# Optimization experiments

Hardware: AMD Instinct MI355X
Metric: run time of the kernel (lower is better)

The kernel has to match this reference:

```python
import jax, jax.numpy as jnp
import numpy as np

N, H, LAT, V = 256, 450, 56, 780  # nodes, hidden_size, latent_size, vocab_size


def _build_tree(seed=0):
    """Random tree on N nodes + DFS path matching the torch dfs() (children in ascending id order)."""
    rng = np.random.default_rng(seed)
    children = [[] for _ in range(N)]
    for i in range(1, N):
        children[int(rng.integers(0, i))].append(i)
    path = []
    stack = [(0, 0)]
    while stack:
        u, ci = stack.pop()
        ch = children[u]
        if ci < len(ch):
            stack.append((u, ci + 1))
            path.append((u, 1))   # descend to child -> stop flag 1
            stack.append((ch[ci], 0))
        else:
            path.append((u, 0))   # backtrack -> stop flag 0
    return path


def setup_inputs() -> dict:
    key = jax.random.key(0)
    ks = jax.random.split(key, 18)
    path = _build_tree()
    L = len(path)  # 2N-1 = 511
    node_ids = np.array([p[0] for p in path], dtype=np.int32)
    stops = np.array([p[1] for p in path], dtype=np.int32)
    next_ids = np.concatenate([node_ids[1:], np.zeros(1, np.int32)])
    label_steps = np.where(stops == 1)[0].astype(np.int32)  # N-1 steps that emit a label
    rng = np.random.default_rng(1)
    vids = rng.integers(0, V, size=N).astype(np.int32)
    node_feature = np.zeros((N, V), np.float32)
    node_feature[np.arange(N), vids] = 1.0  # one-hot vocab features, as in JT-VAE
    real_labels = np.concatenate([vids[:1], vids[next_ids[label_steps]]]).astype(np.int32)  # [N]
    w = lambda k, shape: (jax.random.normal(k, shape, jnp.float32) * 0.05)
    return {
        "latent_code": jax.random.normal(ks[0], (LAT,), jnp.float32),
        "node_feature": jnp.asarray(node_feature),
        "node_ids": jnp.asarray(node_ids),
        "next_ids": jnp.asarray(next_ids),
        "stops": jnp.asarray(stops),
        "label_steps": jnp.asarray(label_steps),
        "real_labels": jnp.asarray(real_labels),
        "Wz_w": w(ks[1], (H, V + H)), "Wz_b": w(ks[2], (H,)),
        "Ur_w": w(ks[3], (H, H)),
        "Wr_w": w(ks[4], (H, V)), "Wr_b": w(ks[5], (H,)),
        "Wh_w": w(ks[6], (H, V + H)), "Wh_b": w(ks[7], (H,)),
        "Wd12_w": w(ks[8], (H, V + LAT)), "Wd12_b": w(ks[9], (H,)),
        "Wd3_w": w(ks[10], (H, H)), "Wd3_b": w(ks[11], (H,)),
        "Ud_w": w(ks[12], (1, 2 * H)), "Ud_b": w(ks[13], (1,)),
        "Wl_w": w(ks[14], (H, H + LAT)), "Wl_b": w(ks[15], (H,)),
        "Ul_w": w(ks[16], (V, H)), "Ul_b": w(ks[17], (V,)),
    }


def reference(latent_code, node_feature, node_ids, next_ids, stops, label_steps, real_labels,
              Wz_w, Wz_b, Ur_w, Wr_w, Wr_b, Wh_w, Wh_b, Wd12_w, Wd12_b, Wd3_w, Wd3_b,
              Ud_w, Ud_b, Wl_w, Wl_b, Ul_w, Ul_b):
    n = node_feature.shape[0]
    h = Wz_w.shape[0]
    L = node_ids.shape[0]

    # Root label: F.relu(U_l(W_l(cat(latent, zeros(h)))))  -- relu OUTSIDE U_l, no softmax.
    root_in = jnp.concatenate([latent_code, jnp.zeros((h,), latent_code.dtype)])
    root_label = jax.nn.relu((root_in @ Wl_w.T + Wl_b) @ Ul_w.T + Ul_b)

    def step(carry, xs):
        hidden, enc = carry            # hidden: [n,n,h], enc: [n,n]
        a, b, is_last = xs
        x = node_feature[a]            # [V] one-hot row
        hs = hidden[:, a]              # [n,h] incoming messages into node a
        # Stop prediction (uses pre-update hidden)
        d12 = jnp.concatenate([x, latent_code]) @ Wd12_w.T + Wd12_b
        d3 = hs.sum(0) @ Wd3_w.T + Wd3_b
        pred_stop = (jax.nn.relu(jnp.concatenate([d12, d3])) @ Ud_w.T + Ud_b)[0]
        # GRU message a -> b, excluding the edge (a,b) from the neighbor mask
        enc0 = enc.at[a, b].set(0.0).at[b, a].set(0.0)
        mask = enc0[:, a]              # [n]
        Hm = hs * mask[:, None]        # masked gathered hidden
        s = Hm.sum(0)                  # [h]
        z = jax.nn.sigmoid(jnp.concatenate([x, s]) @ Wz_w.T + Wz_b)
        r1 = x @ Wr_w.T + Wr_b         # [h]
        r = jax.nn.sigmoid(r1 + Hm @ Ur_w.T)  # [n,h]; torch sums sigmoid over ALL n rows
        gated = jnp.tanh(jnp.concatenate([x, r.sum(0)]) @ Wh_w.T + Wh_b)
        new_h = (1.0 - z) * s + z * gated
        hidden_new = hidden.at[a, b].set(new_h)
        enc_new = enc0.at[a, b].set(1.0).at[b, a].set(1.0)
        hidden = jnp.where(is_last, hidden, hidden_new)  # last path entry: break before update
        enc = jnp.where(is_last, enc, enc_new)
        # Child label: softmax(U_l(relu(W_l(cat(latent, new_h)))))  -- relu INSIDE, then softmax
        lab_in = jnp.concatenate([latent_code, new_h])
        label = jax.nn.softmax(jax.nn.relu(lab_in @ Wl_w.T + Wl_b) @ Ul_w.T + Ul_b)
        return (hidden, enc), (pred_stop, label)

    hidden0 = jnp.zeros((n, n, h), jnp.float32)
    enc0 = jnp.zeros((n, n), jnp.float32)
    is_last = jnp.arange(L) == (L - 1)
    (_, _), (pred_stops, labels) = jax.lax.scan(step, (hidden0, enc0), (node_ids, next_ids, is_last))
    pred_labels = jnp.concatenate([root_label[None], labels[label_steps]], axis=0)  # [N, V]
    return stops.astype(jnp.float32), pred_stops, real_labels, pred_labels
```

## Files before the change

### kernel.cpp

```cpp
#include <hip/hip_runtime.h>
#include <math.h>

#define NN   256
#define HH   450
#define LATD 56
#define VV   780
#define LL   511
#define GSEQ 32
#define TSEQ 512
#define KMAX 15
#define AST  16

typedef float f8 __attribute__((ext_vector_type(8)));

__device__ __forceinline__ float wred_sum(float v) {
    for (int off = 32; off; off >>= 1) v += __shfl_down(v, off, 64);
    return v;
}

__device__ __forceinline__ void aadd(float* p, float v) {
    (void)__hip_atomic_fetch_add(p, v, __ATOMIC_RELAXED, __HIP_MEMORY_SCOPE_AGENT);
}
__device__ __forceinline__ void ast64(unsigned long long* p, unsigned long long v) {
    __hip_atomic_store(p, v, __ATOMIC_RELAXED, __HIP_MEMORY_SCOPE_AGENT);
}
__device__ __forceinline__ unsigned long long ald64(const unsigned long long* p) {
    return __hip_atomic_load(p, __ATOMIC_RELAXED, __HIP_MEMORY_SCOPE_AGENT);
}
__device__ __forceinline__ unsigned long long pk64(float v, unsigned tag) {
    return ((unsigned long long)tag << 32) | (unsigned long long)__float_as_uint(v);
}
__device__ __forceinline__ float lo32f(unsigned long long x) { return __uint_as_float((unsigned)x); }
__device__ __forceinline__ unsigned hi32(unsigned long long x) { return (unsigned)(x >> 32); }

__global__ void k_vid(const float* __restrict__ nf, int* __restrict__ vid) {
    const int u = blockIdx.x;
    for (int v = threadIdx.x; v < VV; v += blockDim.x)
        if (nf[(size_t)u * VV + v] > 0.5f) vid[u] = v;
}

__global__ __launch_bounds__(512) void k_consts(
    const int* __restrict__ vid, const float* __restrict__ latent,
    const float* __restrict__ Wz, const float* __restrict__ Wzb,
    const float* __restrict__ Wr, const float* __restrict__ Wrb,
    const float* __restrict__ Wh, const float* __restrict__ Whb,
    const float* __restrict__ Wd12, const float* __restrict__ Wd12b,
    const float* __restrict__ Ud,
    float* __restrict__ cz, float* __restrict__ r1s, float* __restrict__ sig0,
    float* __restrict__ ch, float* __restrict__ dotd12)
{
    const int u = blockIdx.x, tid = threadIdx.x;
    const int v = vid[u];
    __shared__ float red[8];
    float p = 0.f;
    if (tid < HH) {
        const int i = tid, o = u * HH + i;
        cz[o] = Wz[(size_t)i * (VV + HH) + v] + Wzb[i];
        const float r1 = Wr[(size_t)i * VV + v] + Wrb[i];
        r1s[o] = r1;
        sig0[o] = 1.f / (1.f + expf(-r1));
        ch[o] = Wh[(size_t)i * (VV + HH) + v] + Whb[i];
        float d = Wd12[(size_t)i * (VV + LATD) + v] + Wd12b[i];
        for (int k = 0; k < LATD; ++k)
            d += Wd12[(size_t)i * (VV + LATD) + VV + k] * latent[k];
        p = Ud[i] * fmaxf(d, 0.f);
    }
    p = wred_sum(p);
    if ((tid & 63) == 0) red[tid >> 6] = p;
    __syncthreads();
    if (tid == 0) {
        float s = 0.f;
        for (int w = 0; w < 8; ++w) s += red[w];
        dotd12[u] = s;
    }
}

__global__ __launch_bounds__(512) void k_whsig0(
    const float* __restrict__ Wh, const float* __restrict__ sig0, float* __restrict__ out)
{
    const int u = blockIdx.x, tid = threadIdx.x, wave = tid >> 6, lane = tid & 63;
    __shared__ float sg[HH];
    if (tid < HH) sg[tid] = sig0[u * HH + tid];
    __syncthreads();
    for (int r = wave; r < HH; r += 8) {
        float acc = 0.f;
        for (int k = lane; k < HH; k += 64)
            acc += Wh[(size_t)r * (VV + HH) + VV + k] * sg[k];
        acc = wred_sum(acc);
        if (lane == 0) out[u * HH + r] = acc;
    }
}

__global__ void k_excl(const int* __restrict__ node_ids, const int* __restrict__ next_ids,
                       int* __restrict__ excl, float* __restrict__ ccpre)
{
    const int t = blockIdx.x;
    __shared__ int ex, cnt;
    if (threadIdx.x == 0) { ex = -1; cnt = 0; }
    __syncthreads();
    const int a = node_ids[t], b = next_ids[t];
    for (int tp = threadIdx.x; tp <= t; tp += blockDim.x) {
        if (tp < t && node_ids[tp] == b && next_ids[tp] == a) ex = tp;
        if (tp >= 1 && node_ids[tp] == a) atomicAdd(&cnt, 1);
    }
    __syncthreads();
    if (threadIdx.x == 0) {
        excl[t] = ex;
        ccpre[t] = 256.f - (float)cnt + (ex >= 0 ? 1.f : 0.f);
    }
}

__global__ void k_copy(const int* __restrict__ stops, const int* __restrict__ reall,
                       float* __restrict__ out)
{
    const int i = blockIdx.x * blockDim.x + threadIdx.x;
    if (i < LL) { out[i] = (float)stops[i]; out[LL + i] = 0.f; }
    if (i < NN) out[2 * LL + i] = (float)reall[i];
}

__global__ __launch_bounds__(TSEQ) void k_seq(
    const int* __restrict__ node_ids, const int* __restrict__ excl,
    const float* __restrict__ ccpre,
    const float* __restrict__ Ur, const float* __restrict__ Wz,
    const float* __restrict__ Wh, const float* __restrict__ Wd3,
    const float* __restrict__ Wd3b, const float* __restrict__ Ud,
    const float* __restrict__ Udb,
    const float* __restrict__ cz, const float* __restrict__ r1s,
    const float* __restrict__ ch, const float* __restrict__ WhSig0,
    const float* __restrict__ dotd12,
    float* __restrict__ Wd3SmL,
    float* __restrict__ NewHL, float* __restrict__ WzML, float* __restrict__ WhSvL,
    unsigned long long* __restrict__ bcNh, unsigned long long* __restrict__ bcSig,
    float* __restrict__ pred_out)
{
    const int tid = threadIdx.x, bid = blockIdx.x;
    const int wave = tid >> 6, lane = tid & 63;
    const int kcnt = 14 + (bid < 2 ? 1 : 0);
    const int kbeg = 14 * bid + (bid < 2 ? bid : 2);

    float* myWd3S = Wd3SmL + (size_t)bid * NN * AST;
    float* myNewH = NewHL  + (size_t)bid * LL * AST;
    float* myWzM  = WzML   + (size_t)bid * LL * AST;
    float* myWhSv = WhSvL  + (size_t)bid * LL * AST;

    __shared__ float sSm[NN * AST];
    __shared__ float sWzSm[NN * AST];
    __shared__ float sWhRs[NN * AST];
    __shared__ float nh_full[512];
    __shared__ float sig_full[512];
    __shared__ float sNhR[4][AST];
    __shared__ float sWzR[4][AST];
    __shared__ float sWhR[4][AST];

    f8 urw[2], wzw[2], wd3w[2], whw[2];
    #pragma unroll
    for (int it = 0; it < 2; ++it) {
        const int j = wave + 8 * it;
        const bool vj = j < kcnt;
        const int r = vj ? (kbeg + j) : 0;
        #pragma unroll
        for (int e = 0; e < 8; ++e) {
            const int c = lane + 64 * e;
            const bool vc = vj && (c < HH);
            urw[it][e]  = vc ? Ur[(size_t)r * HH + c] : 0.f;
            wzw[it][e]  = vc ? Wz[(size_t)r * (VV + HH) + VV + c] : 0.f;
            wd3w[it][e] = vc ? Wd3[(size_t)r * HH + c] : 0.f;
            whw[it][e]  = vc ? Wh[(size_t)r * (VV + HH) + VV + c] : 0.f;
        }
    }
    float ud_r = 0.f, w3b_r = 0.f;
    if (tid < kcnt) { ud_r = Ud[HH + kbeg + tid]; w3b_r = Wd3b[kbeg + tid]; }
    const float udb0 = Udb[0];

    for (int i = tid; i < NN * AST; i += TSEQ) { sSm[i] = 0.f; sWzSm[i] = 0.f; sWhRs[i] = 0.f; }
    nh_full[tid] = 0.f; sig_full[tid] = 0.f;

    int ap = node_ids[0];
    float pcz = 0.f, pch = 0.f, pws = 0.f;
    if (tid < kcnt) {
        const int o = ap * HH + kbeg + tid;
        pcz = cz[o]; pch = ch[o]; pws = WhSig0[o];
    }
    float pcc = ccpre[0];
    int  pidx = excl[0];
    __syncthreads();

    for (int t = 1; t <= LL; ++t) {
        const int idx = pidx;
        float nh = 0.f;
        if (tid < kcnt) {
            const int oa = ap * AST + tid;
            float zarg = sWzSm[oa] + pcz;
            float whv  = sWhRs[oa] + pch;
            float sv   = sSm[oa];
            if (idx >= 0) {
                float enh, ewz, ewh;
                if (idx >= t - 4) {
                    const int sl = idx & 3;
                    enh = sNhR[sl][tid]; ewz = sWzR[sl][tid]; ewh = sWhR[sl][tid];
                } else {
                    const int oe = idx * AST + tid;
                    enh = myNewH[oe]; ewz = myWzM[oe]; ewh = myWhSv[oe];
                }
                zarg -= ewz; whv -= ewh; sv -= enh;
            }
            whv += pcc * pws;
            const float z = 1.f / (1.f + expf(-zarg));
            nh = (1.f - z) * sv + z * tanhf(whv);
            if (t < LL)
                ast64(&bcNh[(size_t)((t & 1) * 512 + kbeg + tid)], pk64(nh, (unsigned)t));
            myNewH[(t - 1) * AST + tid] = nh;
            sNhR[(t - 1) & 3][tid] = nh;
        }
        if (wave == 0) {
            float ps = 0.f;
            if (tid < kcnt)
                ps = ud_r * fmaxf(myWd3S[ap * AST + tid] + w3b_r, 0.f);
            ps = wred_sum(ps);
            if (lane == 0) {
                if (bid == 0) ps += dotd12[ap] + udb0;
                aadd(&pred_out[t - 1], ps);
            }
        }
        if (t == LL) break;
        const int a = node_ids[t];
        const unsigned tag = (unsigned)t;
        const int p = t & 1;

        float r1v[2];
        #pragma unroll
        for (int it = 0; it < 2; ++it) {
            const int j = wave + 8 * it;
            r1v[it] = r1s[(size_t)a * HH + ((j < kcnt) ? (kbeg + j) : 0)];
        }
        if (tid < kcnt) sSm[a * AST + tid] += nh;

        if (tid < HH) {
            const unsigned long long* pp = &bcNh[(size_t)(p * 512 + tid)];
            unsigned long long e = ald64(pp);
            while (hi32(e) != tag) { __builtin_amdgcn_s_sleep(1); e = ald64(pp); }
            nh_full[tid] = lo32f(e);
        }
        __syncthreads();

        #pragma unroll
        for (int it = 0; it < 2; ++it) {
            const int j = wave + 8 * it;
            float acc = 0.f;
            #pragma unroll
            for (int e = 0; e < 8; ++e) acc += urw[it][e] * nh_full[lane + 64 * e];
            acc = wred_sum(acc);
            if (lane == 0 && j < kcnt) {
                const float sg = 1.f / (1.f + expf(-(acc + r1v[it])));
                ast64(&bcSig[(size_t)(p * 512 + kbeg + j)], pk64(sg, tag));
            }
        }

        #pragma unroll
        for (int it = 0; it < 2; ++it) {
            const int j = wave + 8 * it;
            float az = 0.f, ad = 0.f;
            #pragma unroll
            for (int e = 0; e < 8; ++e) {
                const float x = nh_full[lane + 64 * e];
                az += wzw[it][e] * x;
                ad += wd3w[it][e] * x;
            }
            az = wred_sum(az); ad = wred_sum(ad);
            if (lane == 0 && j < kcnt) {
                myWzM[(t - 1) * AST + j] = az;
                sWzR[(t - 1) & 3][j] = az;
                sWzSm[a * AST + j] += az;
                myWd3S[a * AST + j] += ad;
            }
        }
        if (tid < kcnt) {
            const int o = a * HH + kbeg + tid;
            pcz = cz[o]; pch = ch[o]; pws = WhSig0[o];
        }
        pcc = ccpre[t]; pidx = excl[t];

        if (tid < HH) {
            const unsigned long long* pp = &bcSig[(size_t)(p * 512 + tid)];
            unsigned long long e = ald64(pp);
            while (hi32(e) != tag) { __builtin_amdgcn_s_sleep(1); e = ald64(pp); }
            sig_full[tid] = lo32f(e);
        }
        __syncthreads();

        #pragma unroll
        for (int it = 0; it < 2; ++it) {
            const int j = wave + 8 * it;
            float aw = 0.f;
            #pragma unroll
            for (int e = 0; e < 8; ++e) aw += whw[it][e] * sig_full[lane + 64 * e];
            aw = wred_sum(aw);
            if (lane == 0 && j < kcnt) {
                myWhSv[(t - 1) * AST + j] = aw;
                sWhR[(t - 1) & 3][j] = aw;
                sWhRs[a * AST + j] += aw;
            }
        }
        ap = a;
        __syncthreads();
    }
}

__global__ __launch_bounds__(512) void k_label(
    const float* __restrict__ latent, const int* __restrict__ lsteps,
    const float* __restrict__ NewHL,
    const float* __restrict__ Wl, const float* __restrict__ Wlb,
    const float* __restrict__ Ul, const float* __restrict__ Ulb,
    float* __restrict__ out)
{
    const int q = blockIdx.x, tid = threadIdx.x, wave = tid >> 6, lane = tid & 63;
    __shared__ float inp[LATD + HH];
    __shared__ float t2[HH];
    __shared__ float lg[VV];
    __shared__ float red[8];
    if (tid < LATD) inp[tid] = latent[tid];
    if (q == 0) {
        if (tid < HH) inp[LATD + tid] = 0.f;
    } else {
        const int t = lsteps[q - 1];
        if (tid < HH) {
            const int b = (tid < 30) ? (tid / 15) : (2 + (tid - 30) / 14);
            const int j = (tid < 30) ? (tid % 15) : ((tid - 30) % 14);
            inp[LATD + tid] = NewHL[((size_t)b * LL + t) * AST + j];
        }
    }
    __syncthreads();
    for (int r = wave; r < HH; r += 8) {
        float acc = 0.f;
        for (int k = lane; k < LATD + HH; k += 64)
            acc += Wl[(size_t)r * (LATD + HH) + k] * inp[k];
        acc = wred_sum(acc);
        if (lane == 0) {
            const float v = acc + Wlb[r];
            t2[r] = (q == 0) ? v : fmaxf(v, 0.f);
        }
    }
    __syncthreads();
    for (int r = wave; r < VV; r += 8) {
        float acc = 0.f;
        for (int k = lane; k < HH; k += 64) acc += Ul[(size_t)r * HH + k] * t2[k];
        acc = wred_sum(acc);
        if (lane == 0) lg[r] = acc + Ulb[r];
    }
    __syncthreads();
    float* outrow = out + 2 * LL + NN + (size_t)q * VV;
    if (q == 0) {
        for (int i = tid; i < VV; i += 512) outrow[i] = fmaxf(lg[i], 0.f);
        return;
    }
    float mx = -1e30f;
    for (int i = tid; i < VV; i += 512) mx = fmaxf(mx, lg[i]);
    for (int off = 32; off; off >>= 1) mx = fmaxf(mx, __shfl_down(mx, off, 64));
    if (lane == 0) red[wave] = mx;
    __syncthreads();
    if (tid == 0) {
        float m = red[0];
        for (int w = 1; w < 8; ++w) m = fmaxf(m, red[w]);
        red[0] = m;
    }
    __syncthreads();
    const float M = red[0];
    float sum = 0.f;
    for (int i = tid; i < VV; i += 512) { const float e = expf(lg[i] - M); lg[i] = e; sum += e; }
    __syncthreads();
    sum = wred_sum(sum);
    if (lane == 0) red[wave] = sum;
    __syncthreads();
    if (tid == 0) {
        float s = 0.f;
        for (int w = 0; w < 8; ++w) s += red[w];
        red[0] = s;
    }
    __syncthreads();
    const float S = red[0];
    for (int i = tid; i < VV; i += 512) outrow[i] = lg[i] / S;
}

extern "C" void kernel_launch(void* const* d_in, const int* in_sizes, int n_in,
                              void* d_out, int out_size, void* d_ws, size_t ws_size,
                              hipStream_t stream)
{
    const float* latent = (const float*)d_in[0];
    const float* nodef  = (const float*)d_in[1];
    const int* node_ids = (const int*)d_in[2];
    const int* next_ids = (const int*)d_in[3];
    const int* stops    = (const int*)d_in[4];
    const int* lsteps   = (const int*)d_in[5];
    const int* reall    = (const int*)d_in[6];
    const float* Wz   = (const float*)d_in[7];
    const float* Wzb  = (const float*)d_in[8];
    const float* Urw  = (const float*)d_in[9];
    const float* Wr   = (const float*)d_in[10];
    const float* Wrb  = (const float*)d_in[11];
    const float* Wh   = (const float*)d_in[12];
    const float* Whb  = (const float*)d_in[13];
    const float* Wd12 = (const float*)d_in[14];
    const float* Wd12b= (const float*)d_in[15];
    const float* Wd3  = (const float*)d_in[16];
    const float* Wd3b = (const float*)d_in[17];
    const float* Ud   = (const float*)d_in[18];
    const float* Udb  = (const float*)d_in[19];
    const float* Wl   = (const float*)d_in[20];
    const float* Wlb  = (const float*)d_in[21];
    const float* Ul   = (const float*)d_in[22];
    const float* Ulb  = (const float*)d_in[23];
    (void)in_sizes; (void)n_in; (void)out_size; (void)ws_size;
    float* out = (float*)d_out;
    float* W = (float*)d_ws;

    size_t o = 0;
    float* Wd3SmL = W + o; o += (size_t)GSEQ * NN * AST;
    unsigned long long* bcNh  = (unsigned long long*)(W + o); o += 2 * 512 * 2;
    unsigned long long* bcSig = (unsigned long long*)(W + o); o += 2 * 512 * 2;
    const size_t zero_floats = o;
    int*   vid    = (int*)(W + o); o += NN;
    int*   excl   = (int*)(W + o); o += LL + 1;
    float* ccpre  = W + o; o += LL + 1;
    float* cz     = W + o; o += NN * HH;
    float* r1s    = W + o; o += NN * HH;
    float* sig0   = W + o; o += NN * HH;
    float* ch     = W + o; o += NN * HH;
    float* WhSig0 = W + o; o += NN * HH;
    float* dotd12 = W + o; o += NN;
    float* NewHL  = W + o; o += (size_t)GSEQ * LL * AST;
    float* WzML   = W + o; o += (size_t)GSEQ * LL * AST;
    float* WhSvL  = W + o; o += (size_t)GSEQ * LL * AST;

    hipMemsetAsync(W, 0, zero_floats * sizeof(float), stream);
    k_vid   <<<NN, 256, 0, stream>>>(nodef, vid);
    k_consts<<<NN, 512, 0, stream>>>(vid, latent, Wz, Wzb, Wr, Wrb, Wh, Whb,
                                     Wd12, Wd12b, Ud, cz, r1s, sig0, ch, dotd12);
    k_whsig0<<<NN, 512, 0, stream>>>(Wh, sig0, WhSig0);
    k_excl  <<<LL, 256, 0, stream>>>(node_ids, next_ids, excl, ccpre);
    k_copy  <<<2, 256, 0, stream>>>(stops, reall, out);
    k_seq   <<<GSEQ, TSEQ, 0, stream>>>(node_ids, excl, ccpre, Urw, Wz, Wh, Wd3, Wd3b,
                                        Ud, Udb, cz, r1s, ch, WhSig0, dotd12,
                                        Wd3SmL, NewHL, WzML, WhSvL,
                                        bcNh, bcSig,
                                        out + LL);
    k_label <<<NN, 512, 0, stream>>>(latent, lsteps, NewHL, Wl, Wlb, Ul, Ulb, out);
}
```

Measured before the change: 2.522 ms.

## Prefetch excluded-edge state early and replace pred atomics with partial-sum reduction

Within the sequential k_seq loop, the global loads of the excluded edge's stored new_h/Wz/WhSv values now happen one iteration early, right after the step index is known, so they are off the next step's critical path. The per-step atomic add of each block's stop-prediction partial becomes a plain store into a per-block partial buffer. A small k_pred kernel then sums those partials. Launch bounds now declare one block per CU. The prefetch relies on the values being written before the next step reads them, and the change adds one extra kernel launch.

```diff
diff --git a/kernel.cpp b/kernel.cpp
--- a/kernel.cpp
+++ b/kernel.cpp
@@ -18,9 +18,6 @@
     return v;
 }
 
-__device__ __forceinline__ void aadd(float* p, float v) {
-    (void)__hip_atomic_fetch_add(p, v, __ATOMIC_RELAXED, __HIP_MEMORY_SCOPE_AGENT);
-}
 __device__ __forceinline__ void ast64(unsigned long long* p, unsigned long long v) {
     __hip_atomic_store(p, v, __ATOMIC_RELAXED, __HIP_MEMORY_SCOPE_AGENT);
 }
@@ -118,7 +115,17 @@
     if (i < NN) out[2 * LL + i] = (float)reall[i];
 }
 
-__global__ __launch_bounds__(TSEQ) void k_seq(
+__global__ void k_pred(const float* __restrict__ pred_part, float* __restrict__ out) {
+    const int t = blockIdx.x * blockDim.x + threadIdx.x;
+    if (t < LL) {
+        float s = 0.f;
+        #pragma unroll 8
+        for (int b = 0; b < GSEQ; ++b) s += pred_part[(size_t)t * GSEQ + b];
+        out[LL + t] = s;
+    }
+}
+
+__global__ __launch_bounds__(TSEQ, 1) void k_seq(
     const int* __restrict__ node_ids, const int* __restrict__ excl,
     const float* __restrict__ ccpre,
     const float* __restrict__ Ur, const float* __restrict__ Wz,
@@ -131,7 +138,7 @@
     float* __restrict__ Wd3SmL,
     float* __restrict__ NewHL, float* __restrict__ WzML, float* __restrict__ WhSvL,
     unsigned long long* __restrict__ bcNh, unsigned long long* __restrict__ bcSig,
-    float* __restrict__ pred_out)
+    float* __restrict__ pred_part)
 {
     const int tid = threadIdx.x, bid = blockIdx.x;
     const int wave = tid >> 6, lane = tid & 63;
@@ -183,6 +190,7 @@
     }
     float pcc = ccpre[0];
     int  pidx = excl[0];
+    float pe_nh = 0.f, pe_wz = 0.f, pe_wh = 0.f;
     __syncthreads();
 
     for (int t = 1; t <= LL; ++t) {
@@ -199,8 +207,7 @@
                     const int sl = idx & 3;
                     enh = sNhR[sl][tid]; ewz = sWzR[sl][tid]; ewh = sWhR[sl][tid];
                 } else {
-                    const int oe = idx * AST + tid;
-                    enh = myNewH[oe]; ewz = myWzM[oe]; ewh = myWhSv[oe];
+                    enh = pe_nh; ewz = pe_wz; ewh = pe_wh;
                 }
                 zarg -= ewz; whv -= ewh; sv -= enh;
             }
@@ -219,7 +226,7 @@
             ps = wred_sum(ps);
             if (lane == 0) {
                 if (bid == 0) ps += dotd12[ap] + udb0;
-                aadd(&pred_out[t - 1], ps);
+                pred_part[(size_t)(t - 1) * GSEQ + bid] = ps;
             }
         }
         if (t == LL) break;
@@ -227,6 +234,12 @@
         const unsigned tag = (unsigned)t;
         const int p = t & 1;
 
+        pidx = excl[t];
+        pe_nh = pe_wz = pe_wh = 0.f;
+        if (pidx >= 0 && pidx < t - 3 && tid < kcnt) {
+            const int oe = pidx * AST + tid;
+            pe_nh = myNewH[oe]; pe_wz = myWzM[oe]; pe_wh = myWhSv[oe];
+        }
         float r1v[2];
         #pragma unroll
         for (int it = 0; it < 2; ++it) {
@@ -278,7 +291,7 @@
             const int o = a * HH + kbeg + tid;
             pcz = cz[o]; pch = ch[o]; pws = WhSig0[o];
         }
-        pcc = ccpre[t]; pidx = excl[t];
+        pcc = ccpre[t];
 
         if (tid < HH) {
             const unsigned long long* pp = &bcSig[(size_t)(p * 512 + tid)];
@@ -430,6 +443,7 @@
     float* NewHL  = W + o; o += (size_t)GSEQ * LL * AST;
     float* WzML   = W + o; o += (size_t)GSEQ * LL * AST;
     float* WhSvL  = W + o; o += (size_t)GSEQ * LL * AST;
+    float* predp  = W + o; o += (size_t)LL * GSEQ;
 
     hipMemsetAsync(W, 0, zero_floats * sizeof(float), stream);
     k_vid   <<<NN, 256, 0, stream>>>(nodef, vid);
@@ -442,6 +456,7 @@
                                         Ud, Udb, cz, r1s, ch, WhSig0, dotd12,
                                         Wd3SmL, NewHL, WzML, WhSvL,
                                         bcNh, bcSig,
-                                        out + LL);
+                                        predp);
+    k_pred  <<<1, 512, 0, stream>>>(predp, out);
     k_label <<<NN, 512, 0, stream>>>(latent, lsteps, NewHL, Wl, Wlb, Ul, Ulb, out);
 }
```

Measured after the change: 2.480 ms. Within noise of the previous version (-1.6%).
